# Optimization experiments

Measured on AMD Instinct MI355X. Metric: run time of the kernel, lower is better.

Reference implementation:

```python
import jax, jax.numpy as jnp
import numpy as np

NEG_SLOPE = 0.2  # PyG GATConv default negative_slope


def _gat_layer(x, src, dst, W_src, W_dst, att_src, att_dst, bias, num_nodes):
    """Single-head GATConv (concat=True, heads=1, add_self_loops=False)."""
    h_src = x @ W_src                      # [N, C]
    h_dst = x @ W_dst                      # [N, C]
    a_src = h_src @ att_src                # [N]
    a_dst = h_dst @ att_dst                # [N]
    # per-edge attention logits: message j -> i uses a_src[j] + a_dst[i]
    e = jax.nn.leaky_relu(a_src[src] + a_dst[dst], NEG_SLOPE)  # [E]
    # numerically stable softmax over incoming edges of each destination
    m = jax.ops.segment_max(e, dst, num_segments=num_nodes)    # [N]
    ee = jnp.exp(e - m[dst])                                   # [E]
    denom = jax.ops.segment_sum(ee, dst, num_segments=num_nodes)  # [N]
    alpha = ee / denom[dst]                                    # [E]
    # attention-weighted scatter-add of source messages
    out = jax.ops.segment_sum(h_src[src] * alpha[:, None], dst,
                              num_segments=num_nodes)          # [N, C]
    return out + bias


def setup_inputs() -> dict:
    key = jax.random.key(0)
    ks = jax.random.split(key, 12)
    N, E, F_IN, HID, OUT = 100000, 1600000, 128, 128, 64
    inp = {
        "x": jax.random.normal(ks[0], (N, F_IN), dtype=jnp.float32),
        "edge_index": jax.random.randint(ks[1], (2, E), 0, N, dtype=jnp.int64
                                         if jax.config.jax_enable_x64 else jnp.int32),
        "W_src1": jax.random.normal(ks[2], (F_IN, HID), dtype=jnp.float32) / np.sqrt(F_IN),
        "W_dst1": jax.random.normal(ks[3], (F_IN, HID), dtype=jnp.float32) / np.sqrt(F_IN),
        "att_src1": jax.random.normal(ks[4], (HID,), dtype=jnp.float32) / np.sqrt(HID),
        "att_dst1": jax.random.normal(ks[5], (HID,), dtype=jnp.float32) / np.sqrt(HID),
        "b1": jnp.zeros((HID,), dtype=jnp.float32),
        "W_src2": jax.random.normal(ks[6], (HID, OUT), dtype=jnp.float32) / np.sqrt(HID),
        "W_dst2": jax.random.normal(ks[7], (HID, OUT), dtype=jnp.float32) / np.sqrt(HID),
        "att_src2": jax.random.normal(ks[8], (OUT,), dtype=jnp.float32) / np.sqrt(OUT),
        "att_dst2": jax.random.normal(ks[9], (OUT,), dtype=jnp.float32) / np.sqrt(OUT),
        "b2": jnp.zeros((OUT,), dtype=jnp.float32),
    }
    return inp


def reference(x, edge_index, W_src1, W_dst1, att_src1, att_dst1, b1,
              W_src2, W_dst2, att_src2, att_dst2, b2):
    N = x.shape[0]
    src, dst = edge_index[0], edge_index[1]
    h = _gat_layer(x, src, dst, W_src1, W_dst1, att_src1, att_dst1, b1, N)
    h = jax.nn.relu(h)
    out = _gat_layer(h, src, dst, W_src2, W_dst2, att_src2, att_dst2, b2, N)
    return out
```

## Files before the change

### kernel.cpp

```cpp
#include <hip/hip_runtime.h>

#define F_IN 128
#define NEG_SLOPE 0.2f
#define SCAN_CHUNK 2048

typedef __attribute__((ext_vector_type(8))) short bf16x8;
typedef __attribute__((ext_vector_type(4))) float f32x4;

__device__ inline unsigned short f2bf(float f) {
    unsigned int u = __float_as_uint(f);
    unsigned int r = (u + 0x7fffu + ((u >> 16) & 1u)) >> 16;
    return (unsigned short)r;
}
__device__ inline float bf2f(unsigned short h) { return __uint_as_float((unsigned int)h << 16); }
__device__ inline float bflo(unsigned int u) { return __uint_as_float(u << 16); }
__device__ inline float bfhi(unsigned int u) { return __uint_as_float(u & 0xffff0000u); }

__device__ inline int bswiz(int n, int k) {
    int ct = n >> 4, rlo = n & 15, kk = k >> 5, q = (k >> 3) & 3, j = k & 7;
    return (((ct * 4 + kk) * 64 + q * 16 + rlo) << 3) + j;
}

__global__ void k_prep(const float* __restrict__ Ws1, const float* __restrict__ Wd1,
                       const float* __restrict__ as1, const float* __restrict__ ad1,
                       const float* __restrict__ Ws2, const float* __restrict__ Wd2,
                       const float* __restrict__ as2, const float* __restrict__ ad2,
                       float* __restrict__ vecs, int* __restrict__ cnt,
                       unsigned short* __restrict__ w1hi, unsigned short* __restrict__ w1lo,
                       unsigned short* __restrict__ w2hi, unsigned short* __restrict__ w2lo,
                       int N) {
    int bid = blockIdx.x, tid = threadIdx.x;
    int i = bid * 256 + tid;
    if (i < N) cnt[i] = 0;
    if (bid == 0 && tid < 128) {
        int f = tid;
        float s1 = 0.f, d1 = 0.f, s2 = 0.f, d2 = 0.f;
        for (int c = 0; c < 128; ++c) {
            s1 += Ws1[f * 128 + c] * as1[c];
            d1 += Wd1[f * 128 + c] * ad1[c];
        }
        for (int c = 0; c < 64; ++c) {
            s2 += Ws2[f * 64 + c] * as2[c];
            d2 += Wd2[f * 64 + c] * ad2[c];
        }
        vecs[f] = s1; vecs[128 + f] = d1; vecs[256 + f] = s2; vecs[384 + f] = d2;
    } else if (bid >= 1 && bid < 65) {
        int idx = (bid - 1) * 256 + tid;
        int n = idx >> 7, k = idx & 127;
        float w = Ws1[k * 128 + n];
        unsigned short h = f2bf(w);
        int si = bswiz(n, k);
        w1hi[si] = h;
        w1lo[si] = f2bf(w - bf2f(h));
    } else if (bid >= 65 && bid < 97) {
        int idx = (bid - 65) * 256 + tid;
        int n = idx >> 7, k = idx & 127;
        float w = Ws2[k * 64 + n];
        unsigned short h = f2bf(w);
        int si = bswiz(n, k);
        w2hi[si] = h;
        w2lo[si] = f2bf(w - bf2f(h));
    }
}

__global__ void k_hist(const int* __restrict__ dsts, int* __restrict__ cnt,
                       int* __restrict__ rank, int E) {
    int e = blockIdx.x * 256 + threadIdx.x;
    if (e < E) rank[e] = atomicAdd(&cnt[dsts[e]], 1);
}

__global__ void k_blocksum(const int* __restrict__ cnt, int* __restrict__ bsum, int N) {
    __shared__ int sh[256];
    int t = threadIdx.x;
    long long base = (long long)blockIdx.x * SCAN_CHUNK + (long long)t * 8;
    int s = 0;
    #pragma unroll
    for (int k = 0; k < 8; ++k) {
        long long i = base + k;
        if (i < N) s += cnt[i];
    }
    sh[t] = s;
    __syncthreads();
    for (int off = 128; off; off >>= 1) {
        if (t < off) sh[t] += sh[t + off];
        __syncthreads();
    }
    if (t == 0) bsum[blockIdx.x] = sh[0];
}

__global__ void k_scan_bsum(const int* __restrict__ bsum, int* __restrict__ bpre,
                            int nb, int* __restrict__ rowptr, int N) {
    if (threadIdx.x == 0 && blockIdx.x == 0) {
        int off = 0;
        for (int b = 0; b < nb; ++b) { bpre[b] = off; off += bsum[b]; }
        rowptr[N] = off;
    }
}

__global__ void k_scan_chunks(const int* __restrict__ cnt, const int* __restrict__ bpre,
                              int* __restrict__ rowptr, int N) {
    __shared__ int sh[256];
    int t = threadIdx.x;
    long long base = (long long)blockIdx.x * SCAN_CHUNK + (long long)t * 8;
    int loc[8];
    int s = 0;
    #pragma unroll
    for (int k = 0; k < 8; ++k) {
        long long i = base + k;
        int v = (i < N) ? cnt[i] : 0;
        loc[k] = s;
        s += v;
    }
    sh[t] = s;
    __syncthreads();
    for (int off = 1; off < 256; off <<= 1) {
        int tmp = (t >= off) ? sh[t - off] : 0;
        __syncthreads();
        sh[t] += tmp;
        __syncthreads();
    }
    int toff = bpre[blockIdx.x] + sh[t] - s;
    #pragma unroll
    for (int k = 0; k < 8; ++k) {
        long long i = base + k;
        if (i < N) rowptr[i] = toff + loc[k];
    }
}

__global__ void k_place(const int* __restrict__ srcs, const int* __restrict__ dsts,
                        const int* __restrict__ rowptr, const int* __restrict__ rank,
                        int* __restrict__ perm_src, int E) {
    int e = blockIdx.x * 256 + threadIdx.x;
    if (e >= E) return;
    perm_src[rowptr[dsts[e]] + rank[e]] = srcs[e];
}

template <int COLS, bool ABF16>
__launch_bounds__(256)
__global__ void k_gemm_mfma(const void* __restrict__ Xv,
                            const unsigned short* __restrict__ Bh,
                            const unsigned short* __restrict__ Bl,
                            const float* __restrict__ vecs_s,
                            const float* __restrict__ vecs_d,
                            unsigned short* __restrict__ H,
                            float* __restrict__ a_s, float* __restrict__ a_d, int N) {
    int tid = threadIdx.x;
    int wave = tid >> 6, lane = tid & 63;
    int q = lane >> 4, rlo = lane & 15;
    long long wrow0 = (long long)blockIdx.x * 128 + wave * 32;

    bf16x8 Ahi[2][4], Alo[2][4];
    #pragma unroll
    for (int rt = 0; rt < 2; ++rt) {
        long long r = wrow0 + rt * 16 + rlo;
        long long rr = (r < N) ? r : (long long)(N - 1);
        float ps = 0.f, pd = 0.f;
        #pragma unroll
        for (int kk = 0; kk < 4; ++kk) {
            int k0 = kk * 32 + q * 8;
            float xv[8];
            if constexpr (ABF16) {
                const unsigned short* Xu = (const unsigned short*)Xv;
                bf16x8 av = *(const bf16x8*)(Xu + rr * 128 + k0);
                Ahi[rt][kk] = av;
                #pragma unroll
                for (int j = 0; j < 8; ++j) xv[j] = bf2f((unsigned short)av[j]);
            } else {
                const float* Xf = (const float*)Xv;
                float4 x0 = *(const float4*)(Xf + rr * 128 + k0);
                float4 x1 = *(const float4*)(Xf + rr * 128 + k0 + 4);
                xv[0] = x0.x; xv[1] = x0.y; xv[2] = x0.z; xv[3] = x0.w;
                xv[4] = x1.x; xv[5] = x1.y; xv[6] = x1.z; xv[7] = x1.w;
                bf16x8 ah, al;
                #pragma unroll
                for (int j = 0; j < 8; ++j) {
                    unsigned short h = f2bf(xv[j]);
                    ah[j] = (short)h;
                    al[j] = (short)f2bf(xv[j] - bf2f(h));
                }
                Ahi[rt][kk] = ah; Alo[rt][kk] = al;
            }
            float4 vs0 = *(const float4*)(vecs_s + k0);
            float4 vs1 = *(const float4*)(vecs_s + k0 + 4);
            float4 vd0 = *(const float4*)(vecs_d + k0);
            float4 vd1 = *(const float4*)(vecs_d + k0 + 4);
            ps += xv[0] * vs0.x + xv[1] * vs0.y + xv[2] * vs0.z + xv[3] * vs0.w
                + xv[4] * vs1.x + xv[5] * vs1.y + xv[6] * vs1.z + xv[7] * vs1.w;
            pd += xv[0] * vd0.x + xv[1] * vd0.y + xv[2] * vd0.z + xv[3] * vd0.w
                + xv[4] * vd1.x + xv[5] * vd1.y + xv[6] * vd1.z + xv[7] * vd1.w;
        }
        ps += __shfl_xor(ps, 16); ps += __shfl_xor(ps, 32);
        pd += __shfl_xor(pd, 16); pd += __shfl_xor(pd, 32);
        if (q == 0 && r < N) { a_s[r] = ps; a_d[r] = pd; }
    }

    const bf16x8* Bh8 = (const bf16x8*)Bh;
    const bf16x8* Bl8 = (const bf16x8*)Bl;
    #pragma unroll 1
    for (int ct = 0; ct < COLS / 16; ++ct) {
        bf16x8 bh[4], bl[4];
        #pragma unroll
        for (int kk = 0; kk < 4; ++kk) {
            bh[kk] = Bh8[(ct * 4 + kk) * 64 + lane];
            bl[kk] = Bl8[(ct * 4 + kk) * 64 + lane];
        }
        f32x4 acc0 = {0.f, 0.f, 0.f, 0.f};
        f32x4 acc1 = {0.f, 0.f, 0.f, 0.f};
        #pragma unroll
        for (int kk = 0; kk < 4; ++kk) {
            acc0 = __builtin_amdgcn_mfma_f32_16x16x32_bf16(Ahi[0][kk], bh[kk], acc0, 0, 0, 0);
            acc1 = __builtin_amdgcn_mfma_f32_16x16x32_bf16(Ahi[1][kk], bh[kk], acc1, 0, 0, 0);
            if constexpr (!ABF16) {
                acc0 = __builtin_amdgcn_mfma_f32_16x16x32_bf16(Alo[0][kk], bh[kk], acc0, 0, 0, 0);
                acc1 = __builtin_amdgcn_mfma_f32_16x16x32_bf16(Alo[1][kk], bh[kk], acc1, 0, 0, 0);
            }
            acc0 = __builtin_amdgcn_mfma_f32_16x16x32_bf16(Ahi[0][kk], bl[kk], acc0, 0, 0, 0);
            acc1 = __builtin_amdgcn_mfma_f32_16x16x32_bf16(Ahi[1][kk], bl[kk], acc1, 0, 0, 0);
        }
        #pragma unroll
        for (int i2 = 0; i2 < 4; ++i2) {
            long long o0 = wrow0 + q * 4 + i2;
            long long o1 = wrow0 + 16 + q * 4 + i2;
            if (o0 < N) H[o0 * COLS + ct * 16 + rlo] = f2bf(acc0[i2]);
            if (o1 < N) H[o1 * COLS + ct * 16 + rlo] = f2bf(acc1[i2]);
        }
    }
}

__launch_bounds__(256)
__global__ void k_agg128(const int* __restrict__ rowptr, const int* __restrict__ perm,
                         const float* __restrict__ a_s, const float* __restrict__ a_d,
                         const unsigned short* __restrict__ H, const float* __restrict__ bias,
                         unsigned short* __restrict__ out_bf, int N) {
    int wave = (int)(((long long)blockIdx.x * 256 + threadIdx.x) >> 6);
    int lane = threadIdx.x & 63;
    if (wave >= N) return;
    int beg = __builtin_amdgcn_readfirstlane(rowptr[wave]);
    int end = __builtin_amdgcn_readfirstlane(rowptr[wave + 1]);
    float ad = __uint_as_float(__builtin_amdgcn_readfirstlane(__float_as_uint(a_d[wave])));

    const unsigned int* H32 = (const unsigned int*)H;
    float acc0 = 0.f, acc1 = 0.f, wsum = 0.f;
    int i = beg;
    for (; i + 8 <= end; i += 8) {
        int s[8];
        unsigned int v[8];
        #pragma unroll
        for (int j = 0; j < 8; ++j)
            s[j] = __builtin_amdgcn_readfirstlane(perm[i + j]);
        #pragma unroll
        for (int j = 0; j < 8; ++j)
            v[j] = H32[(long long)s[j] * 64 + lane];
        #pragma unroll
        for (int j = 0; j < 8; ++j) {
            float t = a_s[s[j]] + ad;
            t = t > 0.f ? t : NEG_SLOPE * t;
            float w = __expf(t);
            acc0 += w * bflo(v[j]);
            acc1 += w * bfhi(v[j]);
            wsum += w;
        }
    }
    for (; i < end; ++i) {
        int s = __builtin_amdgcn_readfirstlane(perm[i]);
        unsigned int v = H32[(long long)s * 64 + lane];
        float t = a_s[s] + ad;
        t = t > 0.f ? t : NEG_SLOPE * t;
        float w = __expf(t);
        acc0 += w * bflo(v); acc1 += w * bfhi(v);
        wsum += w;
    }
    float inv = (wsum > 0.f) ? __fdividef(1.f, wsum) : 0.f;
    float o0 = fmaxf(acc0 * inv + bias[2 * lane], 0.f);
    float o1 = fmaxf(acc1 * inv + bias[2 * lane + 1], 0.f);
    unsigned int pk = (unsigned int)f2bf(o0) | ((unsigned int)f2bf(o1) << 16);
    ((unsigned int*)out_bf)[(long long)wave * 64 + lane] = pk;
}

__launch_bounds__(256)
__global__ void k_agg64(const int* __restrict__ rowptr, const int* __restrict__ perm,
                        const float* __restrict__ a_s, const float* __restrict__ a_d,
                        const unsigned short* __restrict__ H, const float* __restrict__ bias,
                        float* __restrict__ out, int N) {
    int wave = (int)(((long long)blockIdx.x * 256 + threadIdx.x) >> 6);
    int lane = threadIdx.x & 63;
    if (wave >= N) return;
    int c = lane & 31, h = lane >> 5;
    int beg = __builtin_amdgcn_readfirstlane(rowptr[wave]);
    int end = __builtin_amdgcn_readfirstlane(rowptr[wave + 1]);
    float ad = __uint_as_float(__builtin_amdgcn_readfirstlane(__float_as_uint(a_d[wave])));

    const unsigned int* H32 = (const unsigned int*)H;
    float acc0 = 0.f, acc1 = 0.f, wsum = 0.f;
    int base = beg;
    for (; base + 8 <= end; base += 8) {
        int s[4];
        unsigned int v[4];
        #pragma unroll
        for (int j = 0; j < 4; ++j)
            s[j] = perm[base + h + 2 * j];
        #pragma unroll
        for (int j = 0; j < 4; ++j)
            v[j] = H32[(long long)s[j] * 32 + c];
        #pragma unroll
        for (int j = 0; j < 4; ++j) {
            float t = a_s[s[j]] + ad;
            t = t > 0.f ? t : NEG_SLOPE * t;
            float w = __expf(t);
            acc0 += w * bflo(v[j]);
            acc1 += w * bfhi(v[j]);
            wsum += w;
        }
    }
    for (int i = base + h; i < end; i += 2) {
        int s = perm[i];
        unsigned int v = H32[(long long)s * 32 + c];
        float t = a_s[s] + ad;
        t = t > 0.f ? t : NEG_SLOPE * t;
        float w = __expf(t);
        acc0 += w * bflo(v); acc1 += w * bfhi(v);
        wsum += w;
    }
    acc0 += __shfl_xor(acc0, 32);
    acc1 += __shfl_xor(acc1, 32);
    wsum += __shfl_xor(wsum, 32);
    if (h == 0) {
        float inv = (wsum > 0.f) ? __fdividef(1.f, wsum) : 0.f;
        float2 o;
        o.x = acc0 * inv + bias[2 * c];
        o.y = acc1 * inv + bias[2 * c + 1];
        *(float2*)(out + (long long)wave * 64 + 2 * c) = o;
    }
}

extern "C" void kernel_launch(void* const* d_in, const int* in_sizes, int n_in,
                              void* d_out, int out_size, void* d_ws, size_t ws_size,
                              hipStream_t stream) {
    const float* x   = (const float*)d_in[0];
    const int*   ei  = (const int*)d_in[1];
    const float* Ws1 = (const float*)d_in[2];
    const float* Wd1 = (const float*)d_in[3];
    const float* as1 = (const float*)d_in[4];
    const float* ad1 = (const float*)d_in[5];
    const float* b1  = (const float*)d_in[6];
    const float* Ws2 = (const float*)d_in[7];
    const float* Wd2 = (const float*)d_in[8];
    const float* as2 = (const float*)d_in[9];
    const float* ad2 = (const float*)d_in[10];
    const float* b2  = (const float*)d_in[11];
    float* out = (float*)d_out;

    const int N = in_sizes[0] / F_IN;
    const int E = in_sizes[1] / 2;
    const int* srcs = ei;
    const int* dsts = ei + E;

    unsigned short* hbuf = (unsigned short*)d_ws;
    unsigned short* x2bf = hbuf + (size_t)N * 128;
    int*   perm   = (int*)(x2bf + (size_t)N * 128);
    float* a_s1   = (float*)(perm + E);
    float* a_d1   = a_s1 + N;
    float* a_s2   = a_d1 + N;
    float* a_d2   = a_s2 + N;
    int*   cnt    = (int*)(a_d2 + N);
    int*   rowptr = cnt + N;
    int*   bsum   = rowptr + N + 4;
    int*   bpre   = bsum + 64;
    unsigned short* w1hi = (unsigned short*)(bpre + 64);
    unsigned short* w1lo = w1hi + 16384;
    unsigned short* w2hi = w1lo + 16384;
    unsigned short* w2lo = w2hi + 8192;
    float* vecs   = (float*)(w2lo + 8192);
    int*   rank   = (int*)x2bf;

    const int nb = (N + SCAN_CHUNK - 1) / SCAN_CHUNK;

    k_prep<<<(N + 255) / 256, 256, 0, stream>>>(Ws1, Wd1, as1, ad1, Ws2, Wd2,
                                                as2, ad2, vecs, cnt,
                                                w1hi, w1lo, w2hi, w2lo, N);
    k_hist<<<(E + 255) / 256, 256, 0, stream>>>(dsts, cnt, rank, E);
    k_blocksum<<<nb, 256, 0, stream>>>(cnt, bsum, N);
    k_scan_bsum<<<1, 64, 0, stream>>>(bsum, bpre, nb, rowptr, N);
    k_scan_chunks<<<nb, 256, 0, stream>>>(cnt, bpre, rowptr, N);
    k_place<<<(E + 255) / 256, 256, 0, stream>>>(srcs, dsts, rowptr, rank, perm, E);

    k_gemm_mfma<128, false><<<(N + 127) / 128, 256, 0, stream>>>(
        x, w1hi, w1lo, vecs, vecs + 128, hbuf, a_s1, a_d1, N);
    k_agg128<<<(N + 3) / 4, 256, 0, stream>>>(
        rowptr, perm, a_s1, a_d1, hbuf, b1, x2bf, N);

    k_gemm_mfma<64, true><<<(N + 127) / 128, 256, 0, stream>>>(
        x2bf, w2hi, w2lo, vecs + 256, vecs + 384, hbuf, a_s2, a_d2, N);
    k_agg64<<<(N + 3) / 4, 256, 0, stream>>>(
        rowptr, perm, a_s2, a_d2, hbuf, b2, out, N);
}
```

Baseline: 383.6 us.

## Streamline CSR build with cursor atomics and unroll layer-2 aggregation

```diff
diff --git a/kernel.cpp b/kernel.cpp
--- a/kernel.cpp
+++ b/kernel.cpp
@@ -63,10 +63,17 @@
     }
 }
 
-__global__ void k_hist(const int* __restrict__ dsts, int* __restrict__ cnt,
-                       int* __restrict__ rank, int E) {
-    int e = blockIdx.x * 256 + threadIdx.x;
-    if (e < E) rank[e] = atomicAdd(&cnt[dsts[e]], 1);
+__global__ void k_hist(const int* __restrict__ dsts, int* __restrict__ cnt, int E) {
+    int e0 = (blockIdx.x * 256 + threadIdx.x) * 4;
+    if (e0 + 4 <= E) {
+        int4 d4 = *(const int4*)(dsts + e0);
+        atomicAdd(&cnt[d4.x], 1);
+        atomicAdd(&cnt[d4.y], 1);
+        atomicAdd(&cnt[d4.z], 1);
+        atomicAdd(&cnt[d4.w], 1);
+    } else {
+        for (int e = e0; e < E; ++e) atomicAdd(&cnt[dsts[e]], 1);
+    }
 }
 
 __global__ void k_blocksum(const int* __restrict__ cnt, int* __restrict__ bsum, int N) {
@@ -88,20 +95,15 @@
     if (t == 0) bsum[blockIdx.x] = sh[0];
 }
 
-__global__ void k_scan_bsum(const int* __restrict__ bsum, int* __restrict__ bpre,
-                            int nb, int* __restrict__ rowptr, int N) {
-    if (threadIdx.x == 0 && blockIdx.x == 0) {
-        int off = 0;
-        for (int b = 0; b < nb; ++b) { bpre[b] = off; off += bsum[b]; }
-        rowptr[N] = off;
-    }
-}
-
-__global__ void k_scan_chunks(const int* __restrict__ cnt, const int* __restrict__ bpre,
-                              int* __restrict__ rowptr, int N) {
+__global__ void k_scan_chunks(const int* __restrict__ cnt, const int* __restrict__ bsum,
+                              int* __restrict__ rowptr, int* __restrict__ cursor,
+                              int nb, int N) {
     __shared__ int sh[256];
     int t = threadIdx.x;
-    long long base = (long long)blockIdx.x * SCAN_CHUNK + (long long)t * 8;
+    int bid = blockIdx.x;
+    int pre = 0;
+    for (int b = 0; b < bid; ++b) pre += bsum[b];
+    long long base = (long long)bid * SCAN_CHUNK + (long long)t * 8;
     int loc[8];
     int s = 0;
     #pragma unroll
@@ -119,20 +121,25 @@
         sh[t] += tmp;
         __syncthreads();
     }
-    int toff = bpre[blockIdx.x] + sh[t] - s;
+    int toff = pre + sh[t] - s;
     #pragma unroll
     for (int k = 0; k < 8; ++k) {
         long long i = base + k;
-        if (i < N) rowptr[i] = toff + loc[k];
-    }
+        if (i < N) {
+            int val = toff + loc[k];
+            rowptr[i] = val;
+            cursor[i] = val;
+        }
+    }
+    if (bid == nb - 1 && t == 255) rowptr[N] = pre + sh[255];
 }
 
 __global__ void k_place(const int* __restrict__ srcs, const int* __restrict__ dsts,
-                        const int* __restrict__ rowptr, const int* __restrict__ rank,
-                        int* __restrict__ perm_src, int E) {
+                        int* __restrict__ cursor, int* __restrict__ perm_src, int E) {
     int e = blockIdx.x * 256 + threadIdx.x;
     if (e >= E) return;
-    perm_src[rowptr[dsts[e]] + rank[e]] = srcs[e];
+    int pos = atomicAdd(&cursor[dsts[e]], 1);
+    perm_src[pos] = srcs[e];
 }
 
 template <int COLS, bool ABF16>
@@ -293,6 +300,25 @@
     const unsigned int* H32 = (const unsigned int*)H;
     float acc0 = 0.f, acc1 = 0.f, wsum = 0.f;
     int base = beg;
+    for (; base + 16 <= end; base += 16) {
+        int s[8];
+        unsigned int v[8];
+        #pragma unroll
+        for (int j = 0; j < 8; ++j)
+            s[j] = perm[base + h + 2 * j];
+        #pragma unroll
+        for (int j = 0; j < 8; ++j)
+            v[j] = H32[(long long)s[j] * 32 + c];
+        #pragma unroll
+        for (int j = 0; j < 8; ++j) {
+            float t = a_s[s[j]] + ad;
+            t = t > 0.f ? t : NEG_SLOPE * t;
+            float w = __expf(t);
+            acc0 += w * bflo(v[j]);
+            acc1 += w * bfhi(v[j]);
+            wsum += w;
+        }
+    }
     for (; base + 8 <= end; base += 8) {
         int s[4];
         unsigned int v[4];
@@ -364,25 +390,23 @@
     float* a_d2   = a_s2 + N;
     int*   cnt    = (int*)(a_d2 + N);
     int*   rowptr = cnt + N;
-    int*   bsum   = rowptr + N + 4;
-    int*   bpre   = bsum + 64;
-    unsigned short* w1hi = (unsigned short*)(bpre + 64);
+    int*   cursor = rowptr + N + 4;
+    int*   bsum   = cursor + N;
+    unsigned short* w1hi = (unsigned short*)(bsum + 64);
     unsigned short* w1lo = w1hi + 16384;
     unsigned short* w2hi = w1lo + 16384;
     unsigned short* w2lo = w2hi + 8192;
     float* vecs   = (float*)(w2lo + 8192);
-    int*   rank   = (int*)x2bf;
 
     const int nb = (N + SCAN_CHUNK - 1) / SCAN_CHUNK;
 
     k_prep<<<(N + 255) / 256, 256, 0, stream>>>(Ws1, Wd1, as1, ad1, Ws2, Wd2,
                                                 as2, ad2, vecs, cnt,
                                                 w1hi, w1lo, w2hi, w2lo, N);
-    k_hist<<<(E + 255) / 256, 256, 0, stream>>>(dsts, cnt, rank, E);
+    k_hist<<<(E / 4 + 255) / 256, 256, 0, stream>>>(dsts, cnt, E);
     k_blocksum<<<nb, 256, 0, stream>>>(cnt, bsum, N);
-    k_scan_bsum<<<1, 64, 0, stream>>>(bsum, bpre, nb, rowptr, N);
-    k_scan_chunks<<<nb, 256, 0, stream>>>(cnt, bpre, rowptr, N);
-    k_place<<<(E + 255) / 256, 256, 0, stream>>>(srcs, dsts, rowptr, rank, perm, E);
+    k_scan_chunks<<<nb, 256, 0, stream>>>(cnt, bsum, rowptr, cursor, nb, N);
+    k_place<<<(E + 255) / 256, 256, 0, stream>>>(srcs, dsts, cursor, perm, E);
 
     k_gemm_mfma<128, false><<<(N + 127) / 128, 256, 0, stream>>>(
         x, w1hi, w1lo, vecs, vecs + 128, hbuf, a_s1, a_d1, N);
```

Result: slower. 467.0 us (+21.7%).
